# Kernel optimization log

Hardware: AMD Instinct MI355X
Metric: run time of the kernel (lower is better)

Reference implementation:

```python
import jax, jax.numpy as jnp
import numpy as np

B, IN, X, OUT, Z = 4096, 1024, 2048, 512, 6
RES = [False, False, 1, False, 3, False]  # residual_in from init_kwargs
KEEP_P = 0.5  # y: Bernoulli keep-probability for connectivity mask


def _masked_normal(kw, km, shape):
    w = jax.random.normal(kw, shape, dtype=jnp.float32)
    m = jax.random.bernoulli(km, KEEP_P, shape).astype(jnp.float32)
    return w * m


def setup_inputs() -> dict:
    key = jax.random.key(0)
    ks = jax.random.split(key, 40)
    inp = {}
    inp['x'] = jax.random.normal(ks[0], (B, IN), dtype=jnp.float32)
    # weights stored as (in, out) == torch weight.T; mask baked in as in apply_connectivity()
    inp['W_in'] = _masked_normal(ks[1], ks[2], (IN, X))
    inp['b_in'] = jax.random.normal(ks[3], (X,), dtype=jnp.float32)
    hidden_in = [2 * X if RES[i] is not False else X for i in range(Z)]
    for i in range(Z):
        inp[f'Wh{i}'] = _masked_normal(ks[4 + 2 * i], ks[5 + 2 * i], (hidden_in[i], X))
    inp['bh'] = jax.random.normal(ks[20], (Z, X), dtype=jnp.float32)
    inp['W_out'] = _masked_normal(ks[21], ks[22], (X, OUT))
    inp['b_out'] = jax.random.normal(ks[23], (OUT,), dtype=jnp.float32)
    # per-column clip maxima: Poisson(rate=10) as in RandomActivation
    inp['mo_in'] = jax.random.poisson(ks[24], 10.0, (X,)).astype(jnp.float32)
    inp['mo_h'] = jax.random.poisson(ks[25], 10.0, (Z, X)).astype(jnp.float32)
    inp['mo_out'] = jax.random.poisson(ks[26], 10.0, (OUT,)).astype(jnp.float32)
    # per-column activation function ids in [0,5)
    inp['aid_in'] = jax.random.randint(ks[27], (X,), 0, 5, dtype=jnp.int32)
    inp['aid_h'] = jax.random.randint(ks[28], (Z, X), 0, 5, dtype=jnp.int32)
    inp['aid_out'] = jax.random.randint(ks[29], (OUT,), 0, 5, dtype=jnp.int32)
    return inp


def _rand_act(v, aid, mo):
    # fused per-column activation select (RandomActivation) + clip
    acts = [jax.nn.relu(v), jax.nn.sigmoid(v), jnp.tanh(v),
            jnp.where(v >= 0, v, 0.1 * v),  # LeakyReLU(0.1)
            jax.nn.selu(v)]
    out = jnp.select([aid == k for k in range(5)], acts, acts[0])
    return jnp.minimum(out, mo)


def reference(x, W_in, b_in, Wh0, Wh1, Wh2, Wh3, Wh4, Wh5, bh,
              W_out, b_out, mo_in, mo_h, mo_out, aid_in, aid_h, aid_out):
    Ws = [Wh0, Wh1, Wh2, Wh3, Wh4, Wh5]
    h = _rand_act(x @ W_in + b_in, aid_in, mo_in)
    outs = [h]  # temp_outputs
    for i in range(Z):
        if RES[i] is False:
            t = outs[i]
        else:
            t = jnp.concatenate([outs[i], outs[RES[i]]], axis=-1)
        outs.append(_rand_act(t @ Ws[i] + bh[i], aid_h[i], mo_h[i]))
    return _rand_act(outs[-1] @ W_out + b_out, aid_out, mo_out)
```

## Files before the change

### kernel.cpp

```cpp
#include <hip/hip_runtime.h>
#include <stdint.h>
#include <string.h>

#define BDIM   4096
#define INDIM  1024
#define XDIM   2048
#define OUTDIM 512
#define MCH    (BDIM / 16)

#define LO_SCALE 2048.0f
#define INV_LO_SCALE (1.0f / 2048.0f)

typedef _Float16 f16x8 __attribute__((ext_vector_type(8)));
typedef float f32x4 __attribute__((ext_vector_type(4)));

__device__ __forceinline__ unsigned short h2u(_Float16 h) {
  unsigned short u;
  memcpy(&u, &h, 2);
  return u;
}

__device__ __forceinline__ void split_h(float v, unsigned short& h,
                                        unsigned short& l) {
  _Float16 hh = (_Float16)v;
  float r = v - (float)hh;
  _Float16 ll = (_Float16)(r * LO_SCALE);
  h = h2u(hh);
  l = h2u(ll);
}

__device__ __forceinline__ void gld_lds16(const void* g, void* l) {
  __builtin_amdgcn_global_load_lds(
      (const __attribute__((address_space(1))) uint32_t*)g,
      (__attribute__((address_space(3))) uint32_t*)l, 16, 0, 0);
}

__device__ __forceinline__ float rand_act(float v, int a, float mo) {
  float r;
  if (a == 0) {
    r = fmaxf(v, 0.0f);
  } else if (a == 1) {
    r = 1.0f / (1.0f + expf(-v));
  } else if (a == 2) {
    r = tanhf(v);
  } else if (a == 3) {
    r = (v >= 0.0f) ? v : 0.1f * v;
  } else {
    r = (v > 0.0f) ? 1.0507009873554805f * v
                   : 1.7580993408473766f * expm1f(v);
  }
  return fminf(r, mo);
}


__global__ void pack_x(const float* __restrict__ s,
                       unsigned short* __restrict__ dh,
                       unsigned short* __restrict__ dl, int Kin) {
  int ks = blockIdx.x;
  int mblk = blockIdx.y;
  int cc = threadIdx.x >> 6;
  int lane = threadIdx.x & 63;
  int m16 = lane & 15, quad = lane >> 4;
  int row = mblk * 64 + cc * 16 + m16;
  const float* src = s + (size_t)row * Kin + ks * 32 + quad * 8;
  size_t o = ((size_t)ks * MCH + mblk * 4 + cc) * 512 + lane * 8;
#pragma unroll
  for (int j = 0; j < 8; j++) {
    unsigned short h, l;
    split_h(src[j], h, l);
    dh[o + j] = h;
    dl[o + j] = l;
  }
}

__global__ void pack_w(const float* __restrict__ W,
                       unsigned short* __restrict__ dh,
                       unsigned short* __restrict__ dl, int K, int N) {
  __shared__ float t[32][33];
  int n0 = blockIdx.x * 32, k0 = blockIdx.y * 32;
  int tx = threadIdx.x, ty = threadIdx.y;
#pragma unroll
  for (int i = 0; i < 32; i += 8)
    t[ty + i][tx] = W[(size_t)(k0 + ty + i) * N + n0 + tx];
  __syncthreads();
  int tt = ty * 32 + tx;
  int ci = tt >> 7;
  int rem = tt & 127;
  int lane = rem >> 1;
  int j4 = (rem & 1) * 4;
  int m16 = lane & 15, quad = lane >> 4;
  size_t o = ((size_t)(k0 >> 5) * (N >> 4) + (n0 >> 4) + ci) * 512 +
             lane * 8 + j4;
#pragma unroll
  for (int jj = 0; jj < 4; jj++) {
    float v = t[quad * 8 + j4 + jj][ci * 16 + m16];
    unsigned short h, l;
    split_h(v, h, l);
    dh[o + jj] = h;
    dl[o + jj] = l;
  }
}

template <bool OUT_F16>
__global__ __launch_bounds__(256, 4) void gemm_split_act(
    const short* __restrict__ A1h, const short* __restrict__ A1l,
    const short* __restrict__ A2h, const short* __restrict__ A2l,
    const short* __restrict__ BTh, const short* __restrict__ BTl,
    const float* __restrict__ bias, const float* __restrict__ mo,
    const int* __restrict__ aid, unsigned short* __restrict__ Ch,
    unsigned short* __restrict__ Cl, float* __restrict__ Cf, int N, int K,
    int Ksplit) {
  __shared__ short lA0[8 * 512];
  __shared__ short lA1[8 * 512];

  const int tid = threadIdx.x;
  const int lane = tid & 63;
  const int wave = tid >> 6;
  const int m16 = lane & 15, quad = lane >> 4;

  const int blockN = blockIdx.x * 128;
  const int blockM = blockIdx.y * 64;

  f32x4 acc1[4][2];
  f32x4 acc2[4][2];
#pragma unroll
  for (int i = 0; i < 4; i++)
#pragma unroll
    for (int j = 0; j < 2; j++) {
      acc1[i][j] = (f32x4){0.f, 0.f, 0.f, 0.f};
      acc2[i][j] = (f32x4){0.f, 0.f, 0.f, 0.f};
    }

  const int KSTEPS = K >> 5;
  const int KS1 = Ksplit >> 5;

  auto stageA = [&](int ks, short* dA) {
    const short *ph, *pl;
    int kk;
    if (ks < KS1) { ph = A1h; pl = A1l; kk = ks; }
    else          { ph = A2h; pl = A2l; kk = ks - KS1; }
    size_t base = ((size_t)kk * MCH + (blockM >> 4)) * 512 + lane * 8;
#pragma unroll
    for (int s = 0; s < 2; s++) {
      int g = wave * 2 + s;
      int t = g & 3;
      const short* plane = (g < 4) ? ph : pl;
      gld_lds16(plane + base + t * 512, dA + g * 512);
    }
  };

  auto loadB = [&](int ks, f16x8* bH, f16x8* bL) {
    size_t base =
        ((size_t)ks * (N >> 4) + (blockN >> 4) + wave * 2) * 512 + lane * 8;
    bH[0] = *(const f16x8*)(BTh + base);
    bH[1] = *(const f16x8*)(BTh + base + 512);
    bL[0] = *(const f16x8*)(BTl + base);
    bL[1] = *(const f16x8*)(BTl + base + 512);
  };

  auto compute = [&](const short* sA, const f16x8* bH, const f16x8* bL) {
    f16x8 aH[4];
#pragma unroll
    for (int t = 0; t < 4; t++)
      aH[t] = *(const f16x8*)&sA[t * 512 + lane * 8];
#pragma unroll
    for (int i = 0; i < 4; i++)
#pragma unroll
      for (int j = 0; j < 2; j++)
        acc1[i][j] = __builtin_amdgcn_mfma_f32_16x16x32_f16(aH[i], bH[j],
                                                            acc1[i][j], 0, 0, 0);
#pragma unroll
    for (int i = 0; i < 4; i++)
#pragma unroll
      for (int j = 0; j < 2; j++)
        acc2[i][j] = __builtin_amdgcn_mfma_f32_16x16x32_f16(aH[i], bL[j],
                                                            acc2[i][j], 0, 0, 0);
    f16x8 aL[4];
#pragma unroll
    for (int t = 0; t < 4; t++)
      aL[t] = *(const f16x8*)&sA[(4 + t) * 512 + lane * 8];
#pragma unroll
    for (int i = 0; i < 4; i++)
#pragma unroll
      for (int j = 0; j < 2; j++)
        acc2[i][j] = __builtin_amdgcn_mfma_f32_16x16x32_f16(aL[i], bH[j],
                                                            acc2[i][j], 0, 0, 0);
  };

  f16x8 bH0[2], bL0[2], bH1[2], bL1[2];

  stageA(0, lA0);
  loadB(0, bH0, bL0);
  __syncthreads();

  for (int ks = 0; ks < KSTEPS; ks += 2) {
    stageA(ks + 1, lA1);
    loadB(ks + 1, bH1, bL1);
    compute(lA0, bH0, bL0);
    __syncthreads();
    if (ks + 2 < KSTEPS) {
      stageA(ks + 2, lA0);
      loadB(ks + 2, bH0, bL0);
    }
    compute(lA1, bH1, bL1);
    __syncthreads();
  }

#pragma unroll
  for (int j = 0; j < 2; j++) {
    int col = blockN + wave * 32 + j * 16 + m16;
    float b = bias[col];
    float m = mo[col];
    int a = aid[col];
    size_t kbase = OUT_F16 ? ((size_t)(col >> 5) * MCH) * 512 +
                                 (size_t)((col >> 3) & 3) * 128 + (col & 7)
                           : 0;
#pragma unroll
    for (int i = 0; i < 4; i++) {
#pragma unroll
      for (int r = 0; r < 4; r++) {
        int row = blockM + i * 16 + quad * 4 + r;
        float s = acc1[i][j][r] + acc2[i][j][r] * INV_LO_SCALE;
        float v = rand_act(s + b, a, m);
        if (OUT_F16) {
          unsigned short h, l;
          split_h(v, h, l);
          size_t pidx = kbase + (size_t)(row >> 4) * 512 + (row & 15) * 8;
          Ch[pidx] = h;
          Cl[pidx] = l;
        } else {
          Cf[(size_t)row * N + col] = v;
        }
      }
    }
  }
}

extern "C" void kernel_launch(void* const* d_in, const int* in_sizes, int n_in,
                              void* d_out, int out_size, void* d_ws,
                              size_t ws_size, hipStream_t stream) {
  (void)in_sizes; (void)n_in; (void)out_size; (void)ws_size;

  const float* x     = (const float*)d_in[0];
  const float* W_in  = (const float*)d_in[1];
  const float* b_in  = (const float*)d_in[2];
  const float* Wh[6] = {(const float*)d_in[3], (const float*)d_in[4],
                        (const float*)d_in[5], (const float*)d_in[6],
                        (const float*)d_in[7], (const float*)d_in[8]};
  const float* bh    = (const float*)d_in[9];
  const float* W_out = (const float*)d_in[10];
  const float* b_out = (const float*)d_in[11];
  const float* mo_in = (const float*)d_in[12];
  const float* mo_h  = (const float*)d_in[13];
  const float* mo_out= (const float*)d_in[14];
  const int* aid_in  = (const int*)d_in[15];
  const int* aid_h   = (const int*)d_in[16];
  const int* aid_out = (const int*)d_in[17];

  const int hin[6] = {XDIM, XDIM, 2 * XDIM, XDIM, 2 * XDIM, XDIM};

  char* p = (char*)d_ws;
  auto take = [&](size_t elems) {
    short* q = (short*)p;
    p += elems * 2 * 2;
    return q;
  };
  short* x_s = take((size_t)BDIM * INDIM);
  size_t xpl = (size_t)BDIM * INDIM;
  short* w_in_s = take((size_t)XDIM * INDIM);
  size_t wpl_in = (size_t)XDIM * INDIM;
  short* w_h_s[6];
  size_t wpl_h[6];
  for (int i = 0; i < 6; i++) {
    wpl_h[i] = (size_t)XDIM * hin[i];
    w_h_s[i] = take(wpl_h[i]);
  }
  short* w_out_s = take((size_t)OUTDIM * XDIM);
  size_t wpl_out = (size_t)OUTDIM * XDIM;
  const size_t apl = (size_t)BDIM * XDIM;
  short* actA = take(apl);
  short* actB = take(apl);
  short* actC = take(apl);

  pack_x<<<dim3(INDIM / 32, BDIM / 64), dim3(256), 0, stream>>>(
      x, (unsigned short*)x_s, (unsigned short*)(x_s + xpl), INDIM);
  pack_w<<<dim3(XDIM / 32, INDIM / 32), dim3(32, 8), 0, stream>>>(
      W_in, (unsigned short*)w_in_s, (unsigned short*)(w_in_s + wpl_in), INDIM,
      XDIM);
  for (int i = 0; i < 6; i++)
    pack_w<<<dim3(XDIM / 32, hin[i] / 32), dim3(32, 8), 0, stream>>>(
        Wh[i], (unsigned short*)w_h_s[i],
        (unsigned short*)(w_h_s[i] + wpl_h[i]), hin[i], XDIM);
  pack_w<<<dim3(OUTDIM / 32, XDIM / 32), dim3(32, 8), 0, stream>>>(
      W_out, (unsigned short*)w_out_s, (unsigned short*)(w_out_s + wpl_out),
      XDIM, OUTDIM);

  auto G = [&](const short* A1, size_t a1pl, const short* A2, size_t a2pl,
               const short* W, size_t wpl, const float* bi, const float* m,
               const int* a, short* Cb, float* Cf, int N, int K, int Ks) {
    dim3 grid(N / 128, BDIM / 64);
    const short* A2h = A2;
    const short* A2l = A2 ? A2 + a2pl : nullptr;
    if (Cb)
      gemm_split_act<true><<<grid, 256, 0, stream>>>(
          A1, A1 + a1pl, A2h, A2l, W, W + wpl, bi, m, a, (unsigned short*)Cb,
          (unsigned short*)(Cb + apl), nullptr, N, K, Ks);
    else
      gemm_split_act<false><<<grid, 256, 0, stream>>>(
          A1, A1 + a1pl, A2h, A2l, W, W + wpl, bi, m, a, nullptr, nullptr, Cf,
          N, K, Ks);
  };

  G(x_s, xpl, nullptr, 0, w_in_s, wpl_in, b_in, mo_in, aid_in, actA, nullptr,
    XDIM, INDIM, INDIM);
  G(actA, apl, nullptr, 0, w_h_s[0], wpl_h[0], bh + 0 * XDIM, mo_h + 0 * XDIM,
    aid_h + 0 * XDIM, actB, nullptr, XDIM, XDIM, XDIM);
  G(actB, apl, nullptr, 0, w_h_s[1], wpl_h[1], bh + 1 * XDIM, mo_h + 1 * XDIM,
    aid_h + 1 * XDIM, actC, nullptr, XDIM, XDIM, XDIM);
  G(actC, apl, actB, apl, w_h_s[2], wpl_h[2], bh + 2 * XDIM, mo_h + 2 * XDIM,
    aid_h + 2 * XDIM, actA, nullptr, XDIM, 2 * XDIM, XDIM);
  G(actA, apl, nullptr, 0, w_h_s[3], wpl_h[3], bh + 3 * XDIM, mo_h + 3 * XDIM,
    aid_h + 3 * XDIM, actB, nullptr, XDIM, XDIM, XDIM);
  G(actB, apl, actA, apl, w_h_s[4], wpl_h[4], bh + 4 * XDIM, mo_h + 4 * XDIM,
    aid_h + 4 * XDIM, actC, nullptr, XDIM, 2 * XDIM, XDIM);
  G(actC, apl, nullptr, 0, w_h_s[5], wpl_h[5], bh + 5 * XDIM, mo_h + 5 * XDIM,
    aid_h + 5 * XDIM, actB, nullptr, XDIM, XDIM, XDIM);
  G(actB, apl, nullptr, 0, w_out_s, wpl_out, b_out, mo_out, aid_out, nullptr,
    (float*)d_out, OUTDIM, XDIM, XDIM);
}
```

Baseline: 1.157 ms.

## Triple-buffer LDS GEMM pipeline with register prefetch, block swizzle, vectorized packing

Reworks the GEMM main loop into a three-buffer LDS pipeline. The A fragments for the next step are read from LDS into registers while the current MFMAs run, with explicit vmcnt waits, sched_barriers and s_setprio around the MFMA phases. It also remaps block indices so that consecutive workgroups are spread across XCD-sized groups for better L2 locality, and it lowers launch bounds to 2 waves per SIMD to allow more registers. The pack kernels now use vectorized loads and stores. Possible downsides are lower occupancy, higher register pressure, and fragile hand-counted waitcnt values.

Result: slower. 1.352 ms (+16.8%).

```diff
diff --git a/kernel.cpp b/kernel.cpp
--- a/kernel.cpp
+++ b/kernel.cpp
@@ -13,6 +13,8 @@
 
 typedef _Float16 f16x8 __attribute__((ext_vector_type(8)));
 typedef float f32x4 __attribute__((ext_vector_type(4)));
+typedef unsigned short u16x8 __attribute__((ext_vector_type(8)));
+typedef unsigned short u16x4 __attribute__((ext_vector_type(4)));
 
 __device__ __forceinline__ unsigned short h2u(_Float16 h) {
   unsigned short u;
@@ -64,13 +66,19 @@
   int row = mblk * 64 + cc * 16 + m16;
   const float* src = s + (size_t)row * Kin + ks * 32 + quad * 8;
   size_t o = ((size_t)ks * MCH + mblk * 4 + cc) * 512 + lane * 8;
+  float4 v0 = *(const float4*)src;
+  float4 v1 = *(const float4*)(src + 4);
+  float vs[8] = {v0.x, v0.y, v0.z, v0.w, v1.x, v1.y, v1.z, v1.w};
+  u16x8 vh, vl;
 #pragma unroll
   for (int j = 0; j < 8; j++) {
     unsigned short h, l;
-    split_h(src[j], h, l);
-    dh[o + j] = h;
-    dl[o + j] = l;
-  }
+    split_h(vs[j], h, l);
+    vh[j] = h;
+    vl[j] = l;
+  }
+  *(u16x8*)(dh + o) = vh;
+  *(u16x8*)(dl + o) = vl;
 }
 
 __global__ void pack_w(const float* __restrict__ W,
@@ -91,18 +99,21 @@
   int m16 = lane & 15, quad = lane >> 4;
   size_t o = ((size_t)(k0 >> 5) * (N >> 4) + (n0 >> 4) + ci) * 512 +
              lane * 8 + j4;
+  u16x4 vh, vl;
 #pragma unroll
   for (int jj = 0; jj < 4; jj++) {
     float v = t[quad * 8 + j4 + jj][ci * 16 + m16];
     unsigned short h, l;
     split_h(v, h, l);
-    dh[o + jj] = h;
-    dl[o + jj] = l;
-  }
+    vh[jj] = h;
+    vl[jj] = l;
+  }
+  *(u16x4*)(dh + o) = vh;
+  *(u16x4*)(dl + o) = vl;
 }
 
 template <bool OUT_F16>
-__global__ __launch_bounds__(256, 4) void gemm_split_act(
+__global__ __launch_bounds__(256, 2) void gemm_split_act(
     const short* __restrict__ A1h, const short* __restrict__ A1l,
     const short* __restrict__ A2h, const short* __restrict__ A2l,
     const short* __restrict__ BTh, const short* __restrict__ BTl,
@@ -110,16 +121,21 @@
     const int* __restrict__ aid, unsigned short* __restrict__ Ch,
     unsigned short* __restrict__ Cl, float* __restrict__ Cf, int N, int K,
     int Ksplit) {
-  __shared__ short lA0[8 * 512];
-  __shared__ short lA1[8 * 512];
+  __shared__ short lds0[8 * 512];
+  __shared__ short lds1[8 * 512];
+  __shared__ short lds2[8 * 512];
 
   const int tid = threadIdx.x;
   const int lane = tid & 63;
   const int wave = tid >> 6;
   const int m16 = lane & 15, quad = lane >> 4;
 
-  const int blockN = blockIdx.x * 128;
-  const int blockM = blockIdx.y * 64;
+  const int nwg = gridDim.x * 64;
+  const int lin = blockIdx.y * gridDim.x + blockIdx.x;
+  const int cpx = nwg >> 3;
+  const int virt = (lin & 7) * cpx + (lin >> 3);
+  const int blockN = (virt >> 6) * 128;
+  const int blockM = (virt & 63) * 64;
 
   f32x4 acc1[4][2];
   f32x4 acc2[4][2];
@@ -134,35 +150,46 @@
   const int KSTEPS = K >> 5;
   const int KS1 = Ksplit >> 5;
 
-  auto stageA = [&](int ks, short* dA) {
-    const short *ph, *pl;
-    int kk;
-    if (ks < KS1) { ph = A1h; pl = A1l; kk = ks; }
-    else          { ph = A2h; pl = A2l; kk = ks - KS1; }
-    size_t base = ((size_t)kk * MCH + (blockM >> 4)) * 512 + lane * 8;
+  const short* sAh = A1h;
+  const short* sAl = A1l;
+  const size_t aBase0 = (size_t)(blockM >> 4) * 512 + lane * 8;
+  size_t aOff = aBase0;
+  int stageK = 0;
+  auto stageNext = [&](short* dst) {
 #pragma unroll
     for (int s = 0; s < 2; s++) {
       int g = wave * 2 + s;
-      int t = g & 3;
-      const short* plane = (g < 4) ? ph : pl;
-      gld_lds16(plane + base + t * 512, dA + g * 512);
+      const short* plane = (g < 4) ? sAh : sAl;
+      gld_lds16(plane + aOff + (g & 3) * 512, dst + g * 512);
     }
-  };
-
-  auto loadB = [&](int ks, f16x8* bH, f16x8* bL) {
-    size_t base =
-        ((size_t)ks * (N >> 4) + (blockN >> 4) + wave * 2) * 512 + lane * 8;
-    bH[0] = *(const f16x8*)(BTh + base);
-    bH[1] = *(const f16x8*)(BTh + base + 512);
-    bL[0] = *(const f16x8*)(BTl + base);
-    bL[1] = *(const f16x8*)(BTl + base + 512);
-  };
-
-  auto compute = [&](const short* sA, const f16x8* bH, const f16x8* bL) {
-    f16x8 aH[4];
+    aOff += (size_t)MCH * 512;
+    if (++stageK == KS1) { sAh = A2h; sAl = A2l; aOff = aBase0; }
+  };
+
+  size_t bOff = ((size_t)(blockN >> 4) + wave * 2) * 512 + lane * 8;
+  const size_t bStride = (size_t)N * 32;
+  auto loadBNext = [&](f16x8 (&bH)[2], f16x8 (&bL)[2]) {
+    bH[0] = *(const f16x8*)(BTh + bOff);
+    bH[1] = *(const f16x8*)(BTh + bOff + 512);
+    bL[0] = *(const f16x8*)(BTl + bOff);
+    bL[1] = *(const f16x8*)(BTl + bOff + 512);
+    bOff += bStride;
+  };
+
+  f16x8 a0h[4], a0l[4], a1h[4], a1l[4];
+  f16x8 b0H[2], b0L[2], b1H[2], b1L[2];
+
+  auto ldsRead = [&](const short* src, f16x8 (&aH)[4], f16x8 (&aL)[4]) {
 #pragma unroll
     for (int t = 0; t < 4; t++)
-      aH[t] = *(const f16x8*)&sA[t * 512 + lane * 8];
+      aH[t] = *(const f16x8*)&src[t * 512 + lane * 8];
+#pragma unroll
+    for (int t = 0; t < 4; t++)
+      aL[t] = *(const f16x8*)&src[(4 + t) * 512 + lane * 8];
+  };
+
+  auto ph12 = [&](f16x8 (&aH)[4], f16x8 (&bH)[2], f16x8 (&bL)[2]) {
+    __builtin_amdgcn_s_setprio(1);
 #pragma unroll
     for (int i = 0; i < 4; i++)
 #pragma unroll
@@ -175,36 +202,61 @@
       for (int j = 0; j < 2; j++)
         acc2[i][j] = __builtin_amdgcn_mfma_f32_16x16x32_f16(aH[i], bL[j],
                                                             acc2[i][j], 0, 0, 0);
-    f16x8 aL[4];
-#pragma unroll
-    for (int t = 0; t < 4; t++)
-      aL[t] = *(const f16x8*)&sA[(4 + t) * 512 + lane * 8];
+    __builtin_amdgcn_s_setprio(0);
+  };
+  auto ph3 = [&](f16x8 (&aL)[4], f16x8 (&bH)[2]) {
+    __builtin_amdgcn_s_setprio(1);
 #pragma unroll
     for (int i = 0; i < 4; i++)
 #pragma unroll
       for (int j = 0; j < 2; j++)
         acc2[i][j] = __builtin_amdgcn_mfma_f32_16x16x32_f16(aL[i], bH[j],
                                                             acc2[i][j], 0, 0, 0);
-  };
-
-  f16x8 bH0[2], bL0[2], bH1[2], bL1[2];
-
-  stageA(0, lA0);
-  loadB(0, bH0, bL0);
-  __syncthreads();
-
-  for (int ks = 0; ks < KSTEPS; ks += 2) {
-    stageA(ks + 1, lA1);
-    loadB(ks + 1, bH1, bL1);
-    compute(lA0, bH0, bL0);
-    __syncthreads();
-    if (ks + 2 < KSTEPS) {
-      stageA(ks + 2, lA0);
-      loadB(ks + 2, bH0, bL0);
-    }
-    compute(lA1, bH1, bL1);
-    __syncthreads();
-  }
+    __builtin_amdgcn_s_setprio(0);
+  };
+
+#define SB0 __builtin_amdgcn_sched_barrier(0)
+
+  auto ITER = [&](f16x8 (&aHc)[4], f16x8 (&aLc)[4], f16x8 (&aHn)[4],
+                  f16x8 (&aLn)[4], f16x8 (&bHc)[2], f16x8 (&bLc)[2],
+                  f16x8 (&bHn)[2], f16x8 (&bLn)[2], const short* src,
+                  short* dst, bool doStage) {
+    SB0;
+    ph12(aHc, bHc, bLc);
+    SB0;
+    loadBNext(bHn, bLn);
+    if (doStage) stageNext(dst);
+    SB0;
+    if (doStage)
+      asm volatile("s_waitcnt vmcnt(6)" ::: "memory");
+    else
+      asm volatile("s_waitcnt vmcnt(4)" ::: "memory");
+    __builtin_amdgcn_s_barrier();
+    SB0;
+    ldsRead(src, aHn, aLn);
+    SB0;
+    ph3(aLc, bHc);
+    SB0;
+  };
+
+  stageNext(lds0);
+  loadBNext(b0H, b0L);
+  stageNext(lds1);
+  asm volatile("s_waitcnt vmcnt(6)" ::: "memory");
+  __builtin_amdgcn_s_barrier();
+  SB0;
+  ldsRead(lds0, a0h, a0l);
+
+  short *bs = lds1, *bd = lds2, *bt = lds0;
+  for (int ks = 0; ks <= KSTEPS - 4; ks += 2) {
+    ITER(a0h, a0l, a1h, a1l, b0H, b0L, b1H, b1L, bs, bd, true);
+    ITER(a1h, a1l, a0h, a0l, b1H, b1L, b0H, b0L, bd, bt, true);
+    short* tmp = bs; bs = bt; bt = bd; bd = tmp;
+  }
+  ITER(a0h, a0l, a1h, a1l, b0H, b0L, b1H, b1L, bs, nullptr, false);
+  SB0;
+  ph12(a1h, b1H, b1L);
+  ph3(a1l, b1H);
 
 #pragma unroll
   for (int j = 0; j < 2; j++) {
```
